# Kernel tuning notes

Measured on AMD Instinct MI355X. Metric: run time of the kernel, lower is better.

The kernel has to match this reference:

```python
import jax, jax.numpy as jnp
import numpy as np

B, C, H, W, N = 8, 128, 128, 256, 1024
E1_LAMDA = 1.0
E2_LAMDA = 2.0 / 7.0
EPS = 1e-9


def bilinear_sample(fmap, xs):
    """fmap: (B,C,H,W); xs: (B,N,2) with (x,y) pixel coords -> (B*N, C)."""
    Wd, Hd = fmap.shape[3], fmap.shape[2]
    x = jnp.clip(xs[..., 0], 0.0, Wd - 1.0)
    y = jnp.clip(xs[..., 1], 0.0, Hd - 1.0)
    x0 = jnp.clip(jnp.floor(x).astype(jnp.int32), 0, Wd - 2)
    y0 = jnp.clip(jnp.floor(y).astype(jnp.int32), 0, Hd - 2)
    x1, y1 = x0 + 1, y0 + 1
    wx = (x - x0)[..., None]  # (B,N,1)
    wy = (y - y0)[..., None]
    bidx = jnp.arange(fmap.shape[0])[:, None]  # (B,1) broadcasts with (B,N)
    f00 = fmap[bidx, :, y0, x0]  # (B,N,C)
    f01 = fmap[bidx, :, y0, x1]
    f10 = fmap[bidx, :, y1, x0]
    f11 = fmap[bidx, :, y1, x1]
    out = (f00 * (1 - wx) * (1 - wy) + f01 * wx * (1 - wy)
           + f10 * (1 - wx) * wy + f11 * wx * wy)
    return out.reshape(-1, fmap.shape[1])  # (B*N, C)


def setup_inputs() -> dict:
    key = jax.random.key(0)
    k1, k2, k3, k4 = jax.random.split(key, 4)
    fb = jax.random.normal(k1, (B, C, H, W), dtype=jnp.float32)
    # positive match coords (x in [1,W-2], y in [1,H-2]) so noise stays in-bounds-ish
    ub = jax.random.uniform(k2, (B, N, 2), dtype=jnp.float32) \
         * jnp.array([W - 3.0, H - 3.0], jnp.float32) + 1.0
    noise = jax.random.uniform(k3, (B, N, 2), dtype=jnp.float32, minval=-1.0, maxval=1.0)
    f_t = jax.random.normal(k4, (B * N, C), dtype=jnp.float32)
    return {"fb": fb, "f_t": f_t, "ub": ub, "noise": noise}


def reference(fb, f_t, ub, noise):
    xs = ub + noise                                   # perturbed sample points (B,N,2)
    f_s = bilinear_sample(fb, xs)                     # (BN, C)
    r = f_s - f_t                                     # residual
    # np.gradient-style central differences (one-sided at edges)
    gx = jnp.gradient(fb, axis=3)
    gy = jnp.gradient(fb, axis=2)
    Jx = bilinear_sample(gx, xs)                      # (BN, C)
    Jy = bilinear_sample(gy, xs)
    J = jnp.stack([Jx, Jy], axis=-1)                  # (BN, C, 2)
    Hm = jnp.einsum('nci,ncj->nij', J, J) + EPS * jnp.eye(2, dtype=fb.dtype)
    b = jnp.einsum('nci,nc->ni', J, r)                # (BN, 2)
    # analytic 2x2 inverse
    a_, b_, c_, d_ = Hm[:, 0, 0], Hm[:, 0, 1], Hm[:, 1, 0], Hm[:, 1, 1]
    det = a_ * d_ - b_ * c_
    Hinv = jnp.stack([jnp.stack([d_, -b_], -1),
                      jnp.stack([-c_, a_], -1)], -2) / det[:, None, None]
    miu = xs.reshape(-1, 2) - jnp.einsum('nij,nj->ni', Hinv, b)  # (BN, 2)
    diff = ub.reshape(-1, 2) - miu
    e1 = 0.5 * jnp.sum(jnp.einsum('ni,nij,nj->n', diff, Hm, diff))
    det_c = jnp.clip(det, 1e-16, None)
    e2 = (B * N) * jnp.log(jnp.asarray(2.0 * np.pi, fb.dtype)) - 0.5 * jnp.sum(jnp.log(det_c))
    e = E1_LAMDA * e1 + E2_LAMDA * e2
    return (e, e1, e2)
```

## Files before the change

### kernel.cpp

```cpp
#include <hip/hip_runtime.h>

#define Bq 8
#define Cq 128
#define Hq 128
#define Wq 256
#define Nq 1024
#define BN (Bq * Nq)
#define HWq (Hq * Wq)

#define LOG_2PI 1.8378770664093453f
#define EPSq 1e-9f

#define NGRP 32
#define NBINS (Bq * NGRP)
#define BIN_CAP 1024
#define CCH 8
#define NCHUNK (Cq / CCH)

#define BS_OFF 256
#define H_OFF (BS_OFF + NBINS * BIN_CAP)
#define P2_OFF (H_OFF + NCHUNK * BN * 5)

__global__ void zero_bins(int* __restrict__ bc) { bc[threadIdx.x] = 0; }

__global__ __launch_bounds__(256) void binprep(
    const float* __restrict__ ub, const float* __restrict__ noise,
    int* __restrict__ bc, int* __restrict__ bs)
{
    const int n = blockIdx.x * 256 + threadIdx.x;
    const float xsy = ub[2 * n + 1] + noise[2 * n + 1];
    float y = fminf(fmaxf(xsy, 0.0f), (float)(Hq - 1));
    int y0 = (int)floorf(y); y0 = min(max(y0, 0), Hq - 2);
    const int g = (y0 == 0) ? 0 : ((y0 - 1) >> 2);
    const int bin = (n >> 10) * NGRP + g;
    const int idx = atomicAdd(&bc[bin], 1);
    if (idx < BIN_CAP) bs[bin * BIN_CAP + idx] = n;
}

__global__ __launch_bounds__(512) void gn_binned(
    const float* __restrict__ fb,
    const float* __restrict__ f_t,
    const float* __restrict__ ub,
    const float* __restrict__ noise,
    const int* __restrict__ bc,
    const int* __restrict__ bs,
    float* __restrict__ pH)
{
    __shared__ float tile[8 * 256 * 9];
    const int blk  = blockIdx.x;
    const int bin  = blk >> 4;
    const int chunk = blk & 15;
    const int b = bin >> 5;
    const int g = bin & 31;
    const int t = threadIdx.x;

    {
        const int cr = t >> 3;
        const int i  = cr >> 3;
        const int c  = cr & 7;
        const int fq = t & 7;
        const int row = min(4 * g + i, Hq - 1);
        const float* src = fb +
            (((size_t)b * Cq + chunk * CCH + c) * Hq + row) * Wq;
        #pragma unroll
        for (int k = 0; k < 8; ++k) {
            const int f4 = fq + 8 * k;
            const float4 v = *(const float4*)(src + 4 * f4);
            const int px = 4 * f4;
            tile[(i * 256 + px + 0) * 9 + c] = v.x;
            tile[(i * 256 + px + 1) * 9 + c] = v.y;
            tile[(i * 256 + px + 2) * 9 + c] = v.z;
            tile[(i * 256 + px + 3) * 9 + c] = v.w;
        }
    }
    __syncthreads();

    const int nb = bc[bin];
    const int group = t >> 3;
    const int lc = t & 7;
    const int ch = chunk * CCH + lc;

    for (int s = group; s < nb; s += 64) {
        const int n = bs[bin * BIN_CAP + s];

        const float xsx = ub[2 * n]     + noise[2 * n];
        const float xsy = ub[2 * n + 1] + noise[2 * n + 1];

        float x = fminf(fmaxf(xsx, 0.0f), (float)(Wq - 1));
        float y = fminf(fmaxf(xsy, 0.0f), (float)(Hq - 1));
        int x0 = (int)floorf(x); x0 = min(max(x0, 0), Wq - 2);
        int y0 = (int)floorf(y); y0 = min(max(y0, 0), Hq - 2);
        const int x1 = x0 + 1, y1 = y0 + 1;
        const float wx = x - (float)x0;
        const float wy = y - (float)y0;

        const int xlo0 = max(x0 - 1, 0);
        const int xhi1 = min(x1 + 1, Wq - 1);
        const int ylo0 = max(y0 - 1, 0);
        const int yhi1 = min(y1 + 1, Hq - 1);
        const float sx0 = 1.0f / (float)(x1 - xlo0);
        const float sx1 = 1.0f / (float)(xhi1 - x0);
        const float sy0 = 1.0f / (float)(y1 - ylo0);
        const float sy1 = 1.0f / (float)(yhi1 - y0);

        const int ilo = ylo0 - 4 * g;
        const int i0  = y0   - 4 * g;
        const int i1  = i0 + 1;
        const int ihi = yhi1 - 4 * g;

        #define LD(ii, xx) tile[((ii) * 256 + (xx)) * 9 + lc]
        const float f_lo0 = LD(ilo, x0), f_lo1 = LD(ilo, x1);
        const float f0m = LD(i0, xlo0), f00 = LD(i0, x0);
        const float f01 = LD(i0, x1),   f0p = LD(i0, xhi1);
        const float f1m = LD(i1, xlo0), f10 = LD(i1, x0);
        const float f11 = LD(i1, x1),   f1p = LD(i1, xhi1);
        const float f_hi0 = LD(ihi, x0), f_hi1 = LD(ihi, x1);
        #undef LD

        const float gx00 = (f01 - f0m) * sx0;
        const float gx01 = (f0p - f00) * sx1;
        const float gx10 = (f11 - f1m) * sx0;
        const float gx11 = (f1p - f10) * sx1;
        const float gy00 = (f10 - f_lo0) * sy0;
        const float gy01 = (f11 - f_lo1) * sy0;
        const float gy10 = (f_hi0 - f00) * sy1;
        const float gy11 = (f_hi1 - f01) * sy1;

        const float w00 = (1.0f - wx) * (1.0f - wy);
        const float w01 = wx * (1.0f - wy);
        const float w10 = (1.0f - wx) * wy;
        const float w11 = wx * wy;

        const float fs = f00 * w00 + f01 * w01 + f10 * w10 + f11 * w11;
        const float Jx = gx00 * w00 + gx01 * w01 + gx10 * w10 + gx11 * w11;
        const float Jy = gy00 * w00 + gy01 * w01 + gy10 * w10 + gy11 * w11;
        const float r  = fs - f_t[(size_t)n * Cq + ch];

        float hxx = Jx * Jx;
        float hxy = Jx * Jy;
        float hyy = Jy * Jy;
        float bx  = Jx * r;
        float by  = Jy * r;

        #pragma unroll
        for (int off = 1; off < 8; off <<= 1) {
            hxx += __shfl_xor(hxx, off);
            hxy += __shfl_xor(hxy, off);
            hyy += __shfl_xor(hyy, off);
            bx  += __shfl_xor(bx, off);
            by  += __shfl_xor(by, off);
        }
        if (lc == 0) {
            float* o = pH + ((size_t)chunk * BN + n) * 5;
            o[0] = hxx; o[1] = hxy; o[2] = hyy; o[3] = bx; o[4] = by;
        }
    }
}

__global__ __launch_bounds__(256) void gn_finalA(
    const float* __restrict__ pH,
    const float* __restrict__ ub, const float* __restrict__ noise,
    float* __restrict__ p2)
{
    const int n = blockIdx.x * 256 + threadIdx.x;
    float hxx = 0.0f, hxy = 0.0f, hyy = 0.0f, bx = 0.0f, by = 0.0f;
    #pragma unroll
    for (int k = 0; k < NCHUNK; ++k) {
        const float* o = pH + ((size_t)k * BN + n) * 5;
        hxx += o[0]; hxy += o[1]; hyy += o[2]; bx += o[3]; by += o[4];
    }

    const float ubx = ub[2 * n];
    const float uby = ub[2 * n + 1];
    const float xsx = ubx + noise[2 * n];
    const float xsy = uby + noise[2 * n + 1];

    const float A  = hxx + EPSq;
    const float Bv = hxy;
    const float D  = hyy + EPSq;

    const float det = A * D - Bv * Bv;
    const float inv = 1.0f / det;
    const float hbx = ( D * bx - Bv * by) * inv;
    const float hby = (-Bv * bx + A * by) * inv;
    const float dx = ubx - (xsx - hbx);
    const float dy = uby - (xsy - hby);
    const float quad = A * dx * dx + 2.0f * Bv * dx * dy + D * dy * dy;

    const float detc = fmaxf(det, 1e-16f);
    p2[n]      = 0.5f * quad;
    p2[BN + n] = logf(detc);
}

__global__ __launch_bounds__(1024) void gn_reduce_kernel(
    const float* __restrict__ p2, float* __restrict__ out)
{
    float s1 = 0.0f, s2 = 0.0f;
    for (int i = threadIdx.x; i < BN; i += 1024) {
        s1 += p2[i];
        s2 += p2[BN + i];
    }
    #pragma unroll
    for (int off = 32; off > 0; off >>= 1) {
        s1 += __shfl_down(s1, off);
        s2 += __shfl_down(s2, off);
    }
    __shared__ float l1[16], l2[16];
    const int w = threadIdx.x >> 6;
    if ((threadIdx.x & 63) == 0) { l1[w] = s1; l2[w] = s2; }
    __syncthreads();
    if (threadIdx.x == 0) {
        float e1 = 0.0f, sl = 0.0f;
        #pragma unroll
        for (int i = 0; i < 16; ++i) { e1 += l1[i]; sl += l2[i]; }
        const float e2 = (float)BN * LOG_2PI - 0.5f * sl;
        out[0] = e1 + (2.0f / 7.0f) * e2;
        out[1] = e1;
        out[2] = e2;
    }
}

extern "C" void kernel_launch(void* const* d_in, const int* in_sizes, int n_in,
                              void* d_out, int out_size, void* d_ws, size_t ws_size,
                              hipStream_t stream) {
    const float* fb    = (const float*)d_in[0];
    const float* f_t   = (const float*)d_in[1];
    const float* ub    = (const float*)d_in[2];
    const float* noise = (const float*)d_in[3];
    float* out = (float*)d_out;
    int*   wsi = (int*)d_ws;
    float* wsf = (float*)d_ws;

    int*   bc = wsi;
    int*   bs = wsi + BS_OFF;
    float* pH = wsf + H_OFF;
    float* p2 = wsf + P2_OFF;

    zero_bins<<<1, NBINS, 0, stream>>>(bc);
    binprep<<<BN / 256, 256, 0, stream>>>(ub, noise, bc, bs);
    gn_binned<<<NBINS * NCHUNK, 512, 0, stream>>>(fb, f_t, ub, noise, bc, bs, pH);
    gn_finalA<<<BN / 256, 256, 0, stream>>>(pH, ub, noise, p2);
    gn_reduce_kernel<<<1, 1024, 0, stream>>>(p2, out);
}
```

Baseline: 212.7 us.

## Use 16-row overlapping windows with 4-channel chunks to cut halo reloads

Replaces the 4-row bins (each loading an 8-row tile) with 12-row stride windows that load 16 rows, reducing redundant global reads of the feature map from halo overlap. Tiles now store rows contiguously per channel with 4 channels per block. Perturbed coordinates are precomputed once into a workspace array. Doubling the channel chunk count increases partial-sum writes and reads in the finalize step, and the bin capacity check was removed.

```diff
diff --git a/kernel.cpp b/kernel.cpp
--- a/kernel.cpp
+++ b/kernel.cpp
@@ -11,80 +11,88 @@
 #define LOG_2PI 1.8378770664093453f
 #define EPSq 1e-9f
 
-#define NGRP 32
-#define NBINS (Bq * NGRP)
-#define BIN_CAP 1024
-#define CCH 8
+#define RWIN 16
+#define SWIN 12
+#define NWIN 11
+#define NBINSW (Bq * NWIN)
+#define CAPW 1024
+#define CCH 4
 #define NCHUNK (Cq / CCH)
-
-#define BS_OFF 256
-#define H_OFF (BS_OFF + NBINS * BIN_CAP)
-#define P2_OFF (H_OFF + NCHUNK * BN * 5)
-
-__global__ void zero_bins(int* __restrict__ bc) { bc[threadIdx.x] = 0; }
+#define LROW 257
+
+#define BS_OFF 128
+#define GEOM_OFF (BS_OFF + NBINSW * CAPW)
+#define PH_OFF  (GEOM_OFF + BN * 2)
+#define P2_OFF  (PH_OFF + NCHUNK * BN * 5)
+
+__global__ void zero_bins(int* __restrict__ bc) {
+    if (threadIdx.x < NBINSW) bc[threadIdx.x] = 0;
+}
 
 __global__ __launch_bounds__(256) void binprep(
     const float* __restrict__ ub, const float* __restrict__ noise,
-    int* __restrict__ bc, int* __restrict__ bs)
+    int* __restrict__ bc, int* __restrict__ bs, float* __restrict__ geom)
 {
     const int n = blockIdx.x * 256 + threadIdx.x;
-    const float xsy = ub[2 * n + 1] + noise[2 * n + 1];
+    const float2 u  = ((const float2*)ub)[n];
+    const float2 nz = ((const float2*)noise)[n];
+    const float xsx = u.x + nz.x;
+    const float xsy = u.y + nz.y;
+    ((float2*)geom)[n] = make_float2(xsx, xsy);
+
     float y = fminf(fmaxf(xsy, 0.0f), (float)(Hq - 1));
     int y0 = (int)floorf(y); y0 = min(max(y0, 0), Hq - 2);
-    const int g = (y0 == 0) ? 0 : ((y0 - 1) >> 2);
-    const int bin = (n >> 10) * NGRP + g;
+    const int wi = (y0 == 0) ? 0 : (y0 - 1) / SWIN;
+    const int bin = (n >> 10) * NWIN + wi;
     const int idx = atomicAdd(&bc[bin], 1);
-    if (idx < BIN_CAP) bs[bin * BIN_CAP + idx] = n;
+    bs[bin * CAPW + idx] = n;
 }
 
 __global__ __launch_bounds__(512) void gn_binned(
     const float* __restrict__ fb,
     const float* __restrict__ f_t,
-    const float* __restrict__ ub,
-    const float* __restrict__ noise,
     const int* __restrict__ bc,
     const int* __restrict__ bs,
+    const float* __restrict__ geom,
     float* __restrict__ pH)
 {
-    __shared__ float tile[8 * 256 * 9];
-    const int blk  = blockIdx.x;
-    const int bin  = blk >> 4;
-    const int chunk = blk & 15;
-    const int b = bin >> 5;
-    const int g = bin & 31;
-    const int t = threadIdx.x;
+    __shared__ float tile[RWIN * CCH * LROW];
+    const int wb    = blockIdx.x >> 5;
+    const int chunk = blockIdx.x & 31;
+    const int b  = wb / NWIN;
+    const int wi = wb % NWIN;
+    const int r0 = wi * SWIN;
+    const int t  = threadIdx.x;
 
     {
         const int cr = t >> 3;
-        const int i  = cr >> 3;
-        const int c  = cr & 7;
-        const int fq = t & 7;
-        const int row = min(4 * g + i, Hq - 1);
-        const float* src = fb +
-            (((size_t)b * Cq + chunk * CCH + c) * Hq + row) * Wq;
+        const int slot = cr >> 2;
+        const int c    = cr & 3;
+        const int fq   = t & 7;
+        const int row  = min(r0 + slot, Hq - 1);
+        const float* src = fb + (((size_t)b * Cq + chunk * CCH + c) * Hq + row) * Wq;
+        float* drow = tile + (size_t)(slot * CCH + c) * LROW;
         #pragma unroll
         for (int k = 0; k < 8; ++k) {
             const int f4 = fq + 8 * k;
             const float4 v = *(const float4*)(src + 4 * f4);
-            const int px = 4 * f4;
-            tile[(i * 256 + px + 0) * 9 + c] = v.x;
-            tile[(i * 256 + px + 1) * 9 + c] = v.y;
-            tile[(i * 256 + px + 2) * 9 + c] = v.z;
-            tile[(i * 256 + px + 3) * 9 + c] = v.w;
+            drow[4 * f4 + 0] = v.x;
+            drow[4 * f4 + 1] = v.y;
+            drow[4 * f4 + 2] = v.z;
+            drow[4 * f4 + 3] = v.w;
         }
     }
     __syncthreads();
 
-    const int nb = bc[bin];
-    const int group = t >> 3;
-    const int lc = t & 7;
+    const int nb = bc[wb];
+    const int group = t >> 2;
+    const int lc = t & 3;
     const int ch = chunk * CCH + lc;
 
-    for (int s = group; s < nb; s += 64) {
-        const int n = bs[bin * BIN_CAP + s];
-
-        const float xsx = ub[2 * n]     + noise[2 * n];
-        const float xsy = ub[2 * n + 1] + noise[2 * n + 1];
+    for (int s = group; s < nb; s += 128) {
+        const int n = bs[wb * CAPW + s];
+        const float2 xs = ((const float2*)geom)[n];
+        const float xsx = xs.x, xsy = xs.y;
 
         float x = fminf(fmaxf(xsx, 0.0f), (float)(Wq - 1));
         float y = fminf(fmaxf(xsy, 0.0f), (float)(Hq - 1));
@@ -103,12 +111,12 @@
         const float sy0 = 1.0f / (float)(y1 - ylo0);
         const float sy1 = 1.0f / (float)(yhi1 - y0);
 
-        const int ilo = ylo0 - 4 * g;
-        const int i0  = y0   - 4 * g;
+        const int ilo = ylo0 - r0;
+        const int i0  = y0   - r0;
         const int i1  = i0 + 1;
-        const int ihi = yhi1 - 4 * g;
-
-        #define LD(ii, xx) tile[((ii) * 256 + (xx)) * 9 + lc]
+        const int ihi = yhi1 - r0;
+
+        #define LD(ii, xx) tile[(size_t)((ii) * CCH + lc) * LROW + (xx)]
         const float f_lo0 = LD(ilo, x0), f_lo1 = LD(ilo, x1);
         const float f0m = LD(i0, xlo0), f00 = LD(i0, x0);
         const float f01 = LD(i0, x1),   f0p = LD(i0, xhi1);
@@ -143,7 +151,7 @@
         float by  = Jy * r;
 
         #pragma unroll
-        for (int off = 1; off < 8; off <<= 1) {
+        for (int off = 1; off < 4; off <<= 1) {
             hxx += __shfl_xor(hxx, off);
             hxy += __shfl_xor(hxy, off);
             hyy += __shfl_xor(hyy, off);
@@ -159,7 +167,7 @@
 
 __global__ __launch_bounds__(256) void gn_finalA(
     const float* __restrict__ pH,
-    const float* __restrict__ ub, const float* __restrict__ noise,
+    const float* __restrict__ ub, const float* __restrict__ geom,
     float* __restrict__ p2)
 {
     const int n = blockIdx.x * 256 + threadIdx.x;
@@ -170,10 +178,8 @@
         hxx += o[0]; hxy += o[1]; hyy += o[2]; bx += o[3]; by += o[4];
     }
 
-    const float ubx = ub[2 * n];
-    const float uby = ub[2 * n + 1];
-    const float xsx = ubx + noise[2 * n];
-    const float xsy = uby + noise[2 * n + 1];
+    const float2 u  = ((const float2*)ub)[n];
+    const float2 xs = ((const float2*)geom)[n];
 
     const float A  = hxx + EPSq;
     const float Bv = hxy;
@@ -183,8 +189,8 @@
     const float inv = 1.0f / det;
     const float hbx = ( D * bx - Bv * by) * inv;
     const float hby = (-Bv * bx + A * by) * inv;
-    const float dx = ubx - (xsx - hbx);
-    const float dy = uby - (xsy - hby);
+    const float dx = u.x - (xs.x - hbx);
+    const float dy = u.y - (xs.y - hby);
     const float quad = A * dx * dx + 2.0f * Bv * dx * dy + D * dy * dy;
 
     const float detc = fmaxf(det, 1e-16f);
@@ -231,14 +237,15 @@
     int*   wsi = (int*)d_ws;
     float* wsf = (float*)d_ws;
 
-    int*   bc = wsi;
-    int*   bs = wsi + BS_OFF;
-    float* pH = wsf + H_OFF;
-    float* p2 = wsf + P2_OFF;
-
-    zero_bins<<<1, NBINS, 0, stream>>>(bc);
-    binprep<<<BN / 256, 256, 0, stream>>>(ub, noise, bc, bs);
-    gn_binned<<<NBINS * NCHUNK, 512, 0, stream>>>(fb, f_t, ub, noise, bc, bs, pH);
-    gn_finalA<<<BN / 256, 256, 0, stream>>>(pH, ub, noise, p2);
+    int*   bc   = wsi;
+    int*   bs   = wsi + BS_OFF;
+    float* geom = wsf + GEOM_OFF;
+    float* pH   = wsf + PH_OFF;
+    float* p2   = wsf + P2_OFF;
+
+    zero_bins<<<1, 128, 0, stream>>>(bc);
+    binprep<<<BN / 256, 256, 0, stream>>>(ub, noise, bc, bs, geom);
+    gn_binned<<<NBINSW * NCHUNK, 512, 0, stream>>>(fb, f_t, bc, bs, geom, pH);
+    gn_finalA<<<BN / 256, 256, 0, stream>>>(pH, ub, geom, p2);
     gn_reduce_kernel<<<1, 1024, 0, stream>>>(p2, out);
 }
```

Measured after the change: 219.0 us. 3.0% more time.

## Load feature tile via global_load_lds with XOR-swizzled layout and precompute sample coords

Applied to the files above, without the earlier changes.

The feature-row tile is now loaded straight into LDS with global_load_lds 16-byte transfers. This replaces register float4 loads followed by scattered stores into a padded channel-interleaved layout. The tile becomes channel-major per row with an XOR swizzle on 4-float groups to limit bank conflicts on the gather reads. Perturbed sample coordinates are computed once in binprep and stored to workspace so later kernels read one float2 instead of two arrays. The BIN_CAP bound check on bin writes was also removed, which risks overflow if a bin exceeds capacity.

```diff
diff --git a/kernel.cpp b/kernel.cpp
--- a/kernel.cpp
+++ b/kernel.cpp
@@ -18,59 +18,64 @@
 #define NCHUNK (Cq / CCH)
 
 #define BS_OFF 256
-#define H_OFF (BS_OFF + NBINS * BIN_CAP)
-#define P2_OFF (H_OFF + NCHUNK * BN * 5)
+#define GEOM_OFF (BS_OFF + NBINS * BIN_CAP)
+#define PH_OFF  (GEOM_OFF + BN * 2)
+#define P2_OFF  (PH_OFF + NCHUNK * BN * 5)
+
+__device__ __forceinline__ void glds16(const float* g, float* l) {
+    __builtin_amdgcn_global_load_lds(
+        (const __attribute__((address_space(1))) void*)g,
+        (__attribute__((address_space(3))) void*)l, 16, 0, 0);
+}
 
 __global__ void zero_bins(int* __restrict__ bc) { bc[threadIdx.x] = 0; }
 
 __global__ __launch_bounds__(256) void binprep(
     const float* __restrict__ ub, const float* __restrict__ noise,
-    int* __restrict__ bc, int* __restrict__ bs)
+    int* __restrict__ bc, int* __restrict__ bs, float* __restrict__ geom)
 {
     const int n = blockIdx.x * 256 + threadIdx.x;
-    const float xsy = ub[2 * n + 1] + noise[2 * n + 1];
+    const float2 u  = ((const float2*)ub)[n];
+    const float2 nz = ((const float2*)noise)[n];
+    const float xsx = u.x + nz.x;
+    const float xsy = u.y + nz.y;
+    ((float2*)geom)[n] = make_float2(xsx, xsy);
+
     float y = fminf(fmaxf(xsy, 0.0f), (float)(Hq - 1));
     int y0 = (int)floorf(y); y0 = min(max(y0, 0), Hq - 2);
     const int g = (y0 == 0) ? 0 : ((y0 - 1) >> 2);
     const int bin = (n >> 10) * NGRP + g;
     const int idx = atomicAdd(&bc[bin], 1);
-    if (idx < BIN_CAP) bs[bin * BIN_CAP + idx] = n;
+    bs[bin * BIN_CAP + idx] = n;
 }
 
 __global__ __launch_bounds__(512) void gn_binned(
     const float* __restrict__ fb,
     const float* __restrict__ f_t,
-    const float* __restrict__ ub,
-    const float* __restrict__ noise,
     const int* __restrict__ bc,
     const int* __restrict__ bs,
+    const float* __restrict__ geom,
     float* __restrict__ pH)
 {
-    __shared__ float tile[8 * 256 * 9];
-    const int blk  = blockIdx.x;
-    const int bin  = blk >> 4;
-    const int chunk = blk & 15;
+    __shared__ float tile[64 * 256];
+    const int bin   = blockIdx.x >> 4;
+    const int chunk = blockIdx.x & 15;
     const int b = bin >> 5;
     const int g = bin & 31;
     const int t = threadIdx.x;
 
     {
-        const int cr = t >> 3;
-        const int i  = cr >> 3;
-        const int c  = cr & 7;
-        const int fq = t & 7;
-        const int row = min(4 * g + i, Hq - 1);
-        const float* src = fb +
-            (((size_t)b * Cq + chunk * CCH + c) * Hq + row) * Wq;
+        const int w = t >> 6;
+        const int L = t & 63;
+        const int slot = w;
+        const int row = min(4 * g + slot, Hq - 1);
         #pragma unroll
         for (int k = 0; k < 8; ++k) {
-            const int f4 = fq + 8 * k;
-            const float4 v = *(const float4*)(src + 4 * f4);
-            const int px = 4 * f4;
-            tile[(i * 256 + px + 0) * 9 + c] = v.x;
-            tile[(i * 256 + px + 1) * 9 + c] = v.y;
-            tile[(i * 256 + px + 2) * 9 + c] = v.z;
-            tile[(i * 256 + px + 3) * 9 + c] = v.w;
+            const int c = k;
+            const float* src = fb
+                + (((size_t)b * Cq + chunk * CCH + c) * Hq + row) * Wq
+                + ((L ^ c) << 2);
+            glds16(src, &tile[(w * 8 + k) * 256]);
         }
     }
     __syncthreads();
@@ -82,9 +87,8 @@
 
     for (int s = group; s < nb; s += 64) {
         const int n = bs[bin * BIN_CAP + s];
-
-        const float xsx = ub[2 * n]     + noise[2 * n];
-        const float xsy = ub[2 * n + 1] + noise[2 * n + 1];
+        const float2 xs = ((const float2*)geom)[n];
+        const float xsx = xs.x, xsy = xs.y;
 
         float x = fminf(fmaxf(xsx, 0.0f), (float)(Wq - 1));
         float y = fminf(fmaxf(xsy, 0.0f), (float)(Hq - 1));
@@ -108,7 +112,7 @@
         const int i1  = i0 + 1;
         const int ihi = yhi1 - 4 * g;
 
-        #define LD(ii, xx) tile[((ii) * 256 + (xx)) * 9 + lc]
+        #define LD(ii, xx) tile[((ii) * 8 + lc) * 256 + (((((xx) >> 2) ^ lc) << 2) | ((xx) & 3))]
         const float f_lo0 = LD(ilo, x0), f_lo1 = LD(ilo, x1);
         const float f0m = LD(i0, xlo0), f00 = LD(i0, x0);
         const float f01 = LD(i0, x1),   f0p = LD(i0, xhi1);
@@ -159,7 +163,7 @@
 
 __global__ __launch_bounds__(256) void gn_finalA(
     const float* __restrict__ pH,
-    const float* __restrict__ ub, const float* __restrict__ noise,
+    const float* __restrict__ ub, const float* __restrict__ geom,
     float* __restrict__ p2)
 {
     const int n = blockIdx.x * 256 + threadIdx.x;
@@ -170,10 +174,8 @@
         hxx += o[0]; hxy += o[1]; hyy += o[2]; bx += o[3]; by += o[4];
     }
 
-    const float ubx = ub[2 * n];
-    const float uby = ub[2 * n + 1];
-    const float xsx = ubx + noise[2 * n];
-    const float xsy = uby + noise[2 * n + 1];
+    const float2 u  = ((const float2*)ub)[n];
+    const float2 xs = ((const float2*)geom)[n];
 
     const float A  = hxx + EPSq;
     const float Bv = hxy;
@@ -183,8 +185,8 @@
     const float inv = 1.0f / det;
     const float hbx = ( D * bx - Bv * by) * inv;
     const float hby = (-Bv * bx + A * by) * inv;
-    const float dx = ubx - (xsx - hbx);
-    const float dy = uby - (xsy - hby);
+    const float dx = u.x - (xs.x - hbx);
+    const float dy = u.y - (xs.y - hby);
     const float quad = A * dx * dx + 2.0f * Bv * dx * dy + D * dy * dy;
 
     const float detc = fmaxf(det, 1e-16f);
@@ -231,14 +233,15 @@
     int*   wsi = (int*)d_ws;
     float* wsf = (float*)d_ws;
 
-    int*   bc = wsi;
-    int*   bs = wsi + BS_OFF;
-    float* pH = wsf + H_OFF;
-    float* p2 = wsf + P2_OFF;
+    int*   bc   = wsi;
+    int*   bs   = wsi + BS_OFF;
+    float* geom = wsf + GEOM_OFF;
+    float* pH   = wsf + PH_OFF;
+    float* p2   = wsf + P2_OFF;
 
     zero_bins<<<1, NBINS, 0, stream>>>(bc);
-    binprep<<<BN / 256, 256, 0, stream>>>(ub, noise, bc, bs);
-    gn_binned<<<NBINS * NCHUNK, 512, 0, stream>>>(fb, f_t, ub, noise, bc, bs, pH);
-    gn_finalA<<<BN / 256, 256, 0, stream>>>(pH, ub, noise, p2);
+    binprep<<<BN / 256, 256, 0, stream>>>(ub, noise, bc, bs, geom);
+    gn_binned<<<NBINS * NCHUNK, 512, 0, stream>>>(fb, f_t, bc, bs, geom, pH);
+    gn_finalA<<<BN / 256, 256, 0, stream>>>(pH, ub, geom, p2);
     gn_reduce_kernel<<<1, 1024, 0, stream>>>(p2, out);
 }
```

Result: no change. 213.7 us (+0.5%).
